# Kernel optimization log

Hardware: AMD Instinct MI355X
Metric: run time of the kernel (lower is better)

Reference implementation:

```python
import jax, jax.numpy as jnp
import numpy as np
import math

B, L, H, E, D = 4, 2048, 8, 64, 64
EPS = 1e-6

def _adjust(x):
    # signed power-law (sqrt) then L2-normalize over feature dim
    y = jnp.sign(x) * jnp.sqrt(jnp.abs(x) + EPS)
    return y / (jnp.linalg.norm(y, axis=-1, keepdims=True) + EPS)

def setup_inputs() -> dict:
    key = jax.random.key(0)
    kq, kk, kv, ka = jax.random.split(key, 4)
    queries = jax.random.normal(kq, (B, L, H, E), dtype=jnp.float32)
    keys = jax.random.normal(kk, (B, L, H, E), dtype=jnp.float32)
    values = jax.random.normal(kv, (B, L, H, D), dtype=jnp.float32)
    # TriangularCausalMask: True above the diagonal => masked
    attn_mask = jnp.triu(jnp.ones((1, 1, L, L), dtype=bool), k=1)
    alpha = jax.random.normal(ka, (1,), dtype=jnp.float32) * 0.01
    return {"queries": queries, "keys": keys, "values": values,
            "attn_mask": attn_mask, "alpha": alpha}

def reference(queries, keys, values, attn_mask, alpha):
    Bq, Lq, Hq, Eq = queries.shape
    scale = 1.0 / math.sqrt(Eq)
    # Closed form of torch.autograd.functional.jacobian of
    # sum(einsum('blhe,bshe->bhls', q, k)):
    #   d/dq[b,l,h,e] = sum_s k[b,s,h,e]   (independent of l)
    #   d/dk[b,s,h,e] = sum_l q[b,l,h,e]   (independent of s)
    k_sum = jnp.sum(keys, axis=1, keepdims=True)      # [B,1,H,E]
    q_sum = jnp.sum(queries, axis=1, keepdims=True)   # [B,1,H,E]
    q_adj = _adjust(queries + alpha * k_sum)
    k_adj = _adjust(keys + alpha * q_sum)
    scores = jnp.einsum('blhe,bshe->bhls', q_adj, k_adj)  # [B,H,L,S]
    scores = jnp.where(attn_mask, -jnp.inf, scores)
    A = jax.nn.softmax(scale * scores, axis=-1)  # dropout inactive (eval)
    V = jnp.einsum('bhls,bshd->blhd', A, values)
    return V
```

## Files before the change

### kernel.cpp

```cpp
#include <hip/hip_runtime.h>
#include <hip/hip_bf16.h>
#include <math.h>

#define NB 4
#define NL 2048
#define NH 8
#define NE 64
#define ND 64
#define EPSF 1e-6f
#define CEXP 0.180336881f

typedef __attribute__((ext_vector_type(8))) short bf16x8;
typedef __attribute__((ext_vector_type(4))) short s16x4;
typedef __attribute__((ext_vector_type(4))) float f32x4;

static __device__ __forceinline__ unsigned short bfbits(float x) {
  union { __hip_bfloat16 h; unsigned short u; } c;
  c.h = __float2bfloat16(x);
  return c.u;
}
static __device__ __forceinline__ float sgnsqrt(float x) {
  return x > 0.f ? sqrtf(x + EPSF) : (x < 0.f ? -sqrtf(-x + EPSF) : 0.f);
}

__global__ void sums_kernel(const float* __restrict__ q, const float* __restrict__ k,
                            float* __restrict__ pq, float* __restrict__ pk) {
  int bh = blockIdx.x, lp = blockIdx.y;
  int b = bh >> 3, h = bh & 7;
  int t = threadIdx.x;
  int eq = t & 15, lr = t >> 4;
  int wave = t >> 6, lane = t & 63;
  const float* qp = q + (((size_t)b * NL) * NH + h) * NE + eq * 4;
  const float* kp = k + (((size_t)b * NL) * NH + h) * NE + eq * 4;
  f32x4 aq = {0.f, 0.f, 0.f, 0.f}, ak = {0.f, 0.f, 0.f, 0.f};
#pragma unroll
  for (int i = 0; i < 8; ++i) {
    int l = lp * 128 + i * 16 + lr;
    size_t off = (size_t)l * NH * NE;
    aq += *(const f32x4*)(qp + off);
    ak += *(const f32x4*)(kp + off);
  }
#pragma unroll
  for (int c = 0; c < 4; ++c) {
    aq[c] += __shfl_xor(aq[c], 16, 64); aq[c] += __shfl_xor(aq[c], 32, 64);
    ak[c] += __shfl_xor(ak[c], 16, 64); ak[c] += __shfl_xor(ak[c], 32, 64);
  }
  __shared__ f32x4 sq[4][16], sk[4][16];
  if (lane < 16) { sq[wave][lane] = aq; sk[wave][lane] = ak; }
  __syncthreads();
  if (t < 16) {
    f32x4 s = sq[0][t] + sq[1][t] + sq[2][t] + sq[3][t];
    *(f32x4*)(pq + ((size_t)bh * 16 + lp) * 64 + t * 4) = s;
  } else if (t < 32) {
    int e = t - 16;
    f32x4 s = sk[0][e] + sk[1][e] + sk[2][e] + sk[3][e];
    *(f32x4*)(pk + ((size_t)bh * 16 + e < 0 ? 0 : ((size_t)bh * 16) + 0) * 0 + ((size_t)bh * 16 + lp) * 64 + e * 4) = s;
  }
}

__global__ void prep_kernel(const float* __restrict__ q, const float* __restrict__ k,
                            const float* __restrict__ v,
                            const float* __restrict__ pq, const float* __restrict__ pk,
                            const float* __restrict__ alpha,
                            __hip_bfloat16* __restrict__ qadj, __hip_bfloat16* __restrict__ kadj,
                            __hip_bfloat16* __restrict__ vt) {
  __shared__ float aqs[8][68], aks[8][68];
  __shared__ __hip_bfloat16 tile[64][68];
  int t = threadIdx.x;
  if (blockIdx.x < 1024) {
    int rid0 = blockIdx.x * 64;
    int b = rid0 >> 14;
    {
      int h = t >> 5, j = t & 31;
      const float* pqp = pq + ((size_t)(b * 8 + h) * 16) * 64 + j * 2;
      const float* pkp = pk + ((size_t)(b * 8 + h) * 16) * 64 + j * 2;
      float s0 = 0.f, s1 = 0.f, u0 = 0.f, u1 = 0.f;
#pragma unroll
      for (int lp = 0; lp < 16; ++lp) {
        s0 += pqp[lp * 64]; s1 += pqp[lp * 64 + 1];
        u0 += pkp[lp * 64]; u1 += pkp[lp * 64 + 1];
      }
      float al = alpha[0];
      aqs[h][j * 2] = al * s0; aqs[h][j * 2 + 1] = al * s1;
      aks[h][j * 2] = al * u0; aks[h][j * 2 + 1] = al * u1;
    }
    __syncthreads();
    int eq = t & 15, lr = t >> 4;
#pragma unroll
    for (int p = 0; p < 4; ++p) {
      int rid = rid0 + p * 16 + lr;
      int h = rid & 7, l = (rid >> 3) & 2047;
      f32x4 q4 = *(const f32x4*)(q + (size_t)rid * 64 + eq * 4);
      f32x4 k4 = *(const f32x4*)(k + (size_t)rid * 64 + eq * 4);
      f32x4 xq = q4 + *(const f32x4*)&aks[h][eq * 4];
      f32x4 xk = k4 + *(const f32x4*)&aqs[h][eq * 4];
      float yq[4], yk[4];
      float nq = 0.f, nk = 0.f;
#pragma unroll
      for (int c = 0; c < 4; ++c) {
        yq[c] = sgnsqrt(xq[c]); nq += yq[c] * yq[c];
        yk[c] = sgnsqrt(xk[c]); nk += yk[c] * yk[c];
      }
#pragma unroll
      for (int m = 1; m < 16; m <<= 1) {
        nq += __shfl_xor(nq, m, 16);
        nk += __shfl_xor(nk, m, 16);
      }
      float iq = 1.f / (sqrtf(nq) + EPSF);
      float ik = 1.f / (sqrtf(nk) + EPSF);
      s16x4 uq, uk;
#pragma unroll
      for (int c = 0; c < 4; ++c) {
        uq[c] = (short)bfbits(yq[c] * iq);
        uk[c] = (short)bfbits(yk[c] * ik);
      }
      size_t ooff = ((size_t)(b * 8 + h) * 2048 + l) * 64 + eq * 4;
      *(s16x4*)((char*)qadj + ooff * 2) = uq;
      *(s16x4*)((char*)kadj + ooff * 2) = uk;
    }
  } else {
    int blk = blockIdx.x - 1024;
    int s0 = (blk & 31) * 64;
    int bh = blk >> 5;
    int b = bh >> 3, h = bh & 7;
    {
      int sl = t >> 2, dg = t & 3;
      const float* src = v + (((size_t)b * NL + s0 + sl) * NH + h) * ND + dg * 16;
#pragma unroll
      for (int i = 0; i < 4; ++i) {
        f32x4 f = *(const f32x4*)(src + i * 4);
        tile[sl][dg * 16 + i * 4 + 0] = __float2bfloat16(f[0]);
        tile[sl][dg * 16 + i * 4 + 1] = __float2bfloat16(f[1]);
        tile[sl][dg * 16 + i * 4 + 2] = __float2bfloat16(f[2]);
        tile[sl][dg * 16 + i * 4 + 3] = __float2bfloat16(f[3]);
      }
    }
    __syncthreads();
    {
      int d = t >> 2, sg = t & 3;
      __align__(16) __hip_bfloat16 tmp[16];
#pragma unroll
      for (int i = 0; i < 16; ++i) {
        int c = sg * 16 + i;
        int blk32 = c >> 5, cc = c & 31;
        int cq = cc >> 2, ege = cq >> 1, hi = cq & 1;
        int s_local = blk32 * 32 + hi * 16 + ege * 4 + (cc & 3);
        tmp[i] = tile[s_local][d];
      }
      __hip_bfloat16* dst = vt + ((size_t)bh * ND + d) * NL + s0 + sg * 16;
      *(bf16x8*)(dst) = *(const bf16x8*)&tmp[0];
      *(bf16x8*)(dst + 8) = *(const bf16x8*)&tmp[8];
    }
  }
}

__global__ __launch_bounds__(256) void attn_kernel(const __hip_bfloat16* __restrict__ qadj,
                                                   const __hip_bfloat16* __restrict__ kadj,
                                                   const __hip_bfloat16* __restrict__ vt,
                                                   float* __restrict__ out) {
  __shared__ __align__(16) char lds[49152];
  int bh = blockIdx.x;
  int pairid = blockIdx.y;
  int b = bh >> 3, h = bh & 7;
  int wave = threadIdx.x >> 6, lane = threadIdx.x & 63;
  int qr = lane & 15, eg = lane >> 4;
  const char* kgb = (const char*)(kadj + (size_t)bh * NL * NE);
  const char* vgb = (const char*)(vt + (size_t)bh * ND * NL);
  const char* qgb = (const char*)(qadj + (size_t)bh * NL * NE);

  auto STAGE = [&](int bufsel, int ck) {
    char* dstbase = lds + bufsel * 16384;
    int s0 = ck * 64;
#pragma unroll
    for (int c = 0; c < 4; ++c) {
      int T = (wave * 4 + c) * 1024 + lane * 16;
      const char* src;
      if (T < 8192) {
        int S = T ^ (((T >> 7) & 7) << 4);
        src = kgb + (size_t)s0 * 128 + S;
      } else {
        int T2 = T - 8192;
        int S = T2 ^ (((T2 >> 7) & 7) << 4);
        int d = S >> 7, cc = S & 127;
        src = vgb + ((size_t)d * NL + s0) * 2 + cc;
      }
      __builtin_amdgcn_global_load_lds(
          (const __attribute__((address_space(1))) unsigned int*)src,
          (__attribute__((address_space(3))) unsigned int*)(dstbase + (wave * 4 + c) * 1024),
          16, 0, 0);
    }
  };

#pragma unroll 1
  for (int half = 0; half < 2; ++half) {
    int tile = half ? (31 - pairid) : pairid;
    int t0 = tile * 64;
    int nck = tile + 1;
    int qw0 = t0 + wave * 16;

    bf16x8 qf0 = *(const bf16x8*)(qgb + (size_t)(qw0 + qr) * 128 + eg * 16);
    bf16x8 qf1 = *(const bf16x8*)(qgb + (size_t)(qw0 + qr) * 128 + 64 + eg * 16);

    f32x4 acc[4];
#pragma unroll
    for (int dc = 0; dc < 4; ++dc) acc[dc] = (f32x4){0.f, 0.f, 0.f, 0.f};
    float srun = 0.f;

    if (half) {
      asm volatile("s_waitcnt vmcnt(0)" ::: "memory");
      __builtin_amdgcn_sched_barrier(0);
      __builtin_amdgcn_s_barrier();
    }
    STAGE(0, 0);
    if (nck > 1) STAGE(1, 1);

#pragma unroll 1
    for (int ck = 0; ck < nck; ++ck) {
      if (ck + 1 < nck) asm volatile("s_waitcnt vmcnt(4)" ::: "memory");
      else              asm volatile("s_waitcnt vmcnt(0)" ::: "memory");
      __builtin_amdgcn_sched_barrier(0);
      __builtin_amdgcn_s_barrier();
      __builtin_amdgcn_sched_barrier(0);
      if (ck + 2 < nck) STAGE((ck + 2) % 3, ck + 2);
      char* ldsK = lds + (ck % 3) * 16384;
      char* ldsV = ldsK + 8192;

      float p[4][4];
#pragma unroll
      for (int st = 0; st < 4; ++st) {
        f32x4 a = (f32x4){0.f, 0.f, 0.f, 0.f};
        int row = st * 16 + qr;
        int swz = (row & 7) << 4;
        bf16x8 k0 = *(const bf16x8*)(ldsK + ((row * 128 + eg * 16) ^ swz));
        bf16x8 k1 = *(const bf16x8*)(ldsK + ((row * 128 + 64 + eg * 16) ^ swz));
        a = __builtin_amdgcn_mfma_f32_16x16x32_bf16(k0, qf0, a, 0, 0, 0);
        a = __builtin_amdgcn_mfma_f32_16x16x32_bf16(k1, qf1, a, 0, 0, 0);
#pragma unroll
        for (int r = 0; r < 4; ++r) p[st][r] = a[r];
      }
      if (ck == nck - 1) {
#pragma unroll
        for (int st = 0; st < 4; ++st)
#pragma unroll
          for (int r = 0; r < 4; ++r)
            if (t0 + st * 16 + eg * 4 + r > qw0 + qr) p[st][r] = -1e30f;
      }
#pragma unroll
      for (int st = 0; st < 4; ++st)
#pragma unroll
        for (int r = 0; r < 4; ++r) p[st][r] = exp2f((p[st][r] - 1.0f) * CEXP);
      srun += ((p[0][0] + p[0][1] + p[0][2] + p[0][3]) + (p[1][0] + p[1][1] + p[1][2] + p[1][3])) +
              ((p[2][0] + p[2][1] + p[2][2] + p[2][3]) + (p[3][0] + p[3][1] + p[3][2] + p[3][3]));

#pragma unroll
      for (int pp = 0; pp < 2; ++pp) {
        bf16x8 pb;
#pragma unroll
        for (int j = 0; j < 4; ++j) {
          pb[j] = (short)bfbits(p[2 * pp][j]);
          pb[4 + j] = (short)bfbits(p[2 * pp + 1][j]);
        }
#pragma unroll
        for (int dc = 0; dc < 4; ++dc) {
          int d = dc * 16 + qr;
          bf16x8 vf = *(const bf16x8*)(ldsV + ((d * 128 + pp * 64 + eg * 16) ^ ((d & 7) << 4)));
          acc[dc] = __builtin_amdgcn_mfma_f32_16x16x32_bf16(vf, pb, acc[dc], 0, 0, 0);
        }
      }
    }

    srun += __shfl_xor(srun, 16, 64);
    srun += __shfl_xor(srun, 32, 64);
    float inv = 1.f / srun;
    int l = qw0 + qr;
    float* orow = out + (((size_t)b * NL + l) * NH + h) * ND;
#pragma unroll
    for (int dc = 0; dc < 4; ++dc) *(f32x4*)(orow + dc * 16 + eg * 4) = acc[dc] * inv;
  }
}

extern "C" void kernel_launch(void* const* d_in, const int* in_sizes, int n_in,
                              void* d_out, int out_size, void* d_ws, size_t ws_size,
                              hipStream_t stream) {
  const float* q = (const float*)d_in[0];
  const float* k = (const float*)d_in[1];
  const float* v = (const float*)d_in[2];
  const float* alpha = (const float*)d_in[4];
  float* out = (float*)d_out;
  char* ws = (char*)d_ws;

  __hip_bfloat16* qadj = (__hip_bfloat16*)(ws);
  __hip_bfloat16* kadj = (__hip_bfloat16*)(ws + 8388608);
  __hip_bfloat16* vt   = (__hip_bfloat16*)(ws + 16777216);
  float* pq = (float*)(ws + 25165824);
  float* pk = (float*)(ws + 25165824 + 131072);

  sums_kernel<<<dim3(32, 16), 256, 0, stream>>>(q, k, pq, pk);
  prep_kernel<<<dim3(2048), 256, 0, stream>>>(q, k, v, pq, pk, alpha, qadj, kadj, vt);
  attn_kernel<<<dim3(32, 16), 256, 0, stream>>>(qadj, kadj, vt, out);
}
```

Baseline: 162.8 us.

## Split attention work across key halves per wave with smaller query tiles

Restructures the attention kernel so each block handles a 32-row query tile instead of a pair of 64-row tiles. The four waves are split two by two across query halves and key-chunk halves, and the two key-half partial accumulators and row sums are combined through LDS at the end. The grid grows to four times as many blocks, launched heaviest tile first, LDS shrinks to a double buffer, and launch bounds request higher occupancy. LDS offsets are precomputed per thread. The cost is extra K/V restaging per query row and a full wait at every chunk instead of a three-deep pipeline.

```diff
diff --git a/kernel.cpp b/kernel.cpp
--- a/kernel.cpp
+++ b/kernel.cpp
@@ -54,7 +54,7 @@
   } else if (t < 32) {
     int e = t - 16;
     f32x4 s = sk[0][e] + sk[1][e] + sk[2][e] + sk[3][e];
-    *(f32x4*)(pk + ((size_t)bh * 16 + e < 0 ? 0 : ((size_t)bh * 16) + 0) * 0 + ((size_t)bh * 16 + lp) * 64 + e * 4) = s;
+    *(f32x4*)(pk + ((size_t)bh * 16 + lp) * 64 + e * 4) = s;
   }
 }
 
@@ -154,124 +154,141 @@
   }
 }
 
-__global__ __launch_bounds__(256) void attn_kernel(const __hip_bfloat16* __restrict__ qadj,
-                                                   const __hip_bfloat16* __restrict__ kadj,
-                                                   const __hip_bfloat16* __restrict__ vt,
-                                                   float* __restrict__ out) {
-  __shared__ __align__(16) char lds[49152];
+__global__ __launch_bounds__(256, 5) void attn_kernel(const __hip_bfloat16* __restrict__ qadj,
+                                                      const __hip_bfloat16* __restrict__ kadj,
+                                                      const __hip_bfloat16* __restrict__ vt,
+                                                      float* __restrict__ out) {
+  __shared__ __align__(16) char lds[32768];
   int bh = blockIdx.x;
-  int pairid = blockIdx.y;
+  int tile = 63 - (int)blockIdx.y;
   int b = bh >> 3, h = bh & 7;
   int wave = threadIdx.x >> 6, lane = threadIdx.x & 63;
   int qr = lane & 15, eg = lane >> 4;
+  int qhalf = wave >> 1, shalf = wave & 1;
+  int t0 = tile * 32;
+  int nck = (tile >> 1) + 1;
+  int qw0 = t0 + qhalf * 16;
   const char* kgb = (const char*)(kadj + (size_t)bh * NL * NE);
   const char* vgb = (const char*)(vt + (size_t)bh * ND * NL);
   const char* qgb = (const char*)(qadj + (size_t)bh * NL * NE);
 
+  int koff[2][2], voff[4];
+#pragma unroll
+  for (int st2 = 0; st2 < 2; ++st2) {
+    int row = shalf * 32 + st2 * 16 + qr;
+    int swz = (row & 7) << 4;
+    koff[st2][0] = (row * 128 + eg * 16) ^ swz;
+    koff[st2][1] = (row * 128 + 64 + eg * 16) ^ swz;
+  }
+#pragma unroll
+  for (int dc = 0; dc < 4; ++dc) {
+    int d = dc * 16 + qr;
+    voff[dc] = 8192 + ((d * 128 + shalf * 64 + eg * 16) ^ ((d & 7) << 4));
+  }
+  int src_off[4], dst_off[4];
+#pragma unroll
+  for (int c = 0; c < 4; ++c) {
+    dst_off[c] = (wave * 4 + c) * 1024;
+    if (wave < 2) {
+      int T = (wave * 4 + c) * 1024 + lane * 16;
+      src_off[c] = T ^ (((T >> 7) & 7) << 4);
+    } else {
+      int T2 = ((wave - 2) * 4 + c) * 1024 + lane * 16;
+      int S = T2 ^ (((T2 >> 7) & 7) << 4);
+      src_off[c] = (S >> 7) * (NL * 2) + (S & 127);
+    }
+  }
+  const char* sgb = (wave < 2) ? kgb : vgb;
+  int smul = (wave < 2) ? 8192 : 128;
+
   auto STAGE = [&](int bufsel, int ck) {
-    char* dstbase = lds + bufsel * 16384;
-    int s0 = ck * 64;
-#pragma unroll
-    for (int c = 0; c < 4; ++c) {
-      int T = (wave * 4 + c) * 1024 + lane * 16;
-      const char* src;
-      if (T < 8192) {
-        int S = T ^ (((T >> 7) & 7) << 4);
-        src = kgb + (size_t)s0 * 128 + S;
-      } else {
-        int T2 = T - 8192;
-        int S = T2 ^ (((T2 >> 7) & 7) << 4);
-        int d = S >> 7, cc = S & 127;
-        src = vgb + ((size_t)d * NL + s0) * 2 + cc;
-      }
+    const char* sb = sgb + (size_t)ck * smul;
+    char* db = lds + bufsel * 16384;
+#pragma unroll
+    for (int c = 0; c < 4; ++c)
       __builtin_amdgcn_global_load_lds(
-          (const __attribute__((address_space(1))) unsigned int*)src,
-          (__attribute__((address_space(3))) unsigned int*)(dstbase + (wave * 4 + c) * 1024),
+          (const __attribute__((address_space(1))) unsigned int*)(sb + src_off[c]),
+          (__attribute__((address_space(3))) unsigned int*)(db + dst_off[c]),
           16, 0, 0);
-    }
   };
 
+  bf16x8 qf0 = *(const bf16x8*)(qgb + (size_t)(qw0 + qr) * 128 + eg * 16);
+  bf16x8 qf1 = *(const bf16x8*)(qgb + (size_t)(qw0 + qr) * 128 + 64 + eg * 16);
+
+  f32x4 acc[4];
+#pragma unroll
+  for (int dc = 0; dc < 4; ++dc) acc[dc] = (f32x4){0.f, 0.f, 0.f, 0.f};
+  float srun = 0.f;
+
+  STAGE(0, 0);
 #pragma unroll 1
-  for (int half = 0; half < 2; ++half) {
-    int tile = half ? (31 - pairid) : pairid;
-    int t0 = tile * 64;
-    int nck = tile + 1;
-    int qw0 = t0 + wave * 16;
-
-    bf16x8 qf0 = *(const bf16x8*)(qgb + (size_t)(qw0 + qr) * 128 + eg * 16);
-    bf16x8 qf1 = *(const bf16x8*)(qgb + (size_t)(qw0 + qr) * 128 + 64 + eg * 16);
-
-    f32x4 acc[4];
-#pragma unroll
-    for (int dc = 0; dc < 4; ++dc) acc[dc] = (f32x4){0.f, 0.f, 0.f, 0.f};
-    float srun = 0.f;
-
-    if (half) {
-      asm volatile("s_waitcnt vmcnt(0)" ::: "memory");
-      __builtin_amdgcn_sched_barrier(0);
-      __builtin_amdgcn_s_barrier();
-    }
-    STAGE(0, 0);
-    if (nck > 1) STAGE(1, 1);
-
-#pragma unroll 1
-    for (int ck = 0; ck < nck; ++ck) {
-      if (ck + 1 < nck) asm volatile("s_waitcnt vmcnt(4)" ::: "memory");
-      else              asm volatile("s_waitcnt vmcnt(0)" ::: "memory");
-      __builtin_amdgcn_sched_barrier(0);
-      __builtin_amdgcn_s_barrier();
-      __builtin_amdgcn_sched_barrier(0);
-      if (ck + 2 < nck) STAGE((ck + 2) % 3, ck + 2);
-      char* ldsK = lds + (ck % 3) * 16384;
-      char* ldsV = ldsK + 8192;
-
-      float p[4][4];
-#pragma unroll
-      for (int st = 0; st < 4; ++st) {
-        f32x4 a = (f32x4){0.f, 0.f, 0.f, 0.f};
-        int row = st * 16 + qr;
-        int swz = (row & 7) << 4;
-        bf16x8 k0 = *(const bf16x8*)(ldsK + ((row * 128 + eg * 16) ^ swz));
-        bf16x8 k1 = *(const bf16x8*)(ldsK + ((row * 128 + 64 + eg * 16) ^ swz));
-        a = __builtin_amdgcn_mfma_f32_16x16x32_bf16(k0, qf0, a, 0, 0, 0);
-        a = __builtin_amdgcn_mfma_f32_16x16x32_bf16(k1, qf1, a, 0, 0, 0);
-#pragma unroll
-        for (int r = 0; r < 4; ++r) p[st][r] = a[r];
-      }
-      if (ck == nck - 1) {
-#pragma unroll
-        for (int st = 0; st < 4; ++st)
-#pragma unroll
-          for (int r = 0; r < 4; ++r)
-            if (t0 + st * 16 + eg * 4 + r > qw0 + qr) p[st][r] = -1e30f;
-      }
-#pragma unroll
-      for (int st = 0; st < 4; ++st)
-#pragma unroll
-        for (int r = 0; r < 4; ++r) p[st][r] = exp2f((p[st][r] - 1.0f) * CEXP);
-      srun += ((p[0][0] + p[0][1] + p[0][2] + p[0][3]) + (p[1][0] + p[1][1] + p[1][2] + p[1][3])) +
-              ((p[2][0] + p[2][1] + p[2][2] + p[2][3]) + (p[3][0] + p[3][1] + p[3][2] + p[3][3]));
-
-#pragma unroll
-      for (int pp = 0; pp < 2; ++pp) {
-        bf16x8 pb;
-#pragma unroll
-        for (int j = 0; j < 4; ++j) {
-          pb[j] = (short)bfbits(p[2 * pp][j]);
-          pb[4 + j] = (short)bfbits(p[2 * pp + 1][j]);
-        }
-#pragma unroll
-        for (int dc = 0; dc < 4; ++dc) {
-          int d = dc * 16 + qr;
-          bf16x8 vf = *(const bf16x8*)(ldsV + ((d * 128 + pp * 64 + eg * 16) ^ ((d & 7) << 4)));
-          acc[dc] = __builtin_amdgcn_mfma_f32_16x16x32_bf16(vf, pb, acc[dc], 0, 0, 0);
-        }
-      }
-    }
-
-    srun += __shfl_xor(srun, 16, 64);
-    srun += __shfl_xor(srun, 32, 64);
-    float inv = 1.f / srun;
+  for (int ck = 0; ck < nck; ++ck) {
+    asm volatile("s_waitcnt vmcnt(0)" ::: "memory");
+    __builtin_amdgcn_sched_barrier(0);
+    __builtin_amdgcn_s_barrier();
+    __builtin_amdgcn_sched_barrier(0);
+    if (ck + 1 < nck) STAGE((ck + 1) & 1, ck + 1);
+    char* base = lds + (ck & 1) * 16384;
+
+    float p[2][4];
+#pragma unroll
+    for (int st2 = 0; st2 < 2; ++st2) {
+      f32x4 a = (f32x4){0.f, 0.f, 0.f, 0.f};
+      bf16x8 k0 = *(const bf16x8*)(base + koff[st2][0]);
+      bf16x8 k1 = *(const bf16x8*)(base + koff[st2][1]);
+      a = __builtin_amdgcn_mfma_f32_16x16x32_bf16(k0, qf0, a, 0, 0, 0);
+      a = __builtin_amdgcn_mfma_f32_16x16x32_bf16(k1, qf1, a, 0, 0, 0);
+#pragma unroll
+      for (int r = 0; r < 4; ++r) p[st2][r] = a[r];
+    }
+    if (ck == nck - 1) {
+      int sbase = ck * 64 + shalf * 32 + eg * 4;
+      int qg = qw0 + qr;
+#pragma unroll
+      for (int st2 = 0; st2 < 2; ++st2)
+#pragma unroll
+        for (int r = 0; r < 4; ++r)
+          if (sbase + st2 * 16 + r > qg) p[st2][r] = -1e30f;
+    }
+#pragma unroll
+    for (int st2 = 0; st2 < 2; ++st2)
+#pragma unroll
+      for (int r = 0; r < 4; ++r) p[st2][r] = exp2f((p[st2][r] - 1.0f) * CEXP);
+    srun += ((p[0][0] + p[0][1]) + (p[0][2] + p[0][3])) +
+            ((p[1][0] + p[1][1]) + (p[1][2] + p[1][3]));
+
+    bf16x8 pb;
+#pragma unroll
+    for (int j = 0; j < 4; ++j) {
+      pb[j] = (short)bfbits(p[0][j]);
+      pb[4 + j] = (short)bfbits(p[1][j]);
+    }
+#pragma unroll
+    for (int dc = 0; dc < 4; ++dc) {
+      bf16x8 vf = *(const bf16x8*)(base + voff[dc]);
+      acc[dc] = __builtin_amdgcn_mfma_f32_16x16x32_bf16(vf, pb, acc[dc], 0, 0, 0);
+    }
+  }
+
+  srun += __shfl_xor(srun, 16, 64);
+  srun += __shfl_xor(srun, 32, 64);
+  __syncthreads();
+  if (shalf == 1) {
+    float* m = (float*)(lds + qhalf * 4352 + lane * 68);
+#pragma unroll
+    for (int dc = 0; dc < 4; ++dc)
+#pragma unroll
+      for (int r = 0; r < 4; ++r) m[dc * 4 + r] = acc[dc][r];
+    m[16] = srun;
+  }
+  __syncthreads();
+  if (shalf == 0) {
+    const float* m = (const float*)(lds + qhalf * 4352 + lane * 68);
+#pragma unroll
+    for (int dc = 0; dc < 4; ++dc)
+#pragma unroll
+      for (int r = 0; r < 4; ++r) acc[dc][r] += m[dc * 4 + r];
+    float inv = 1.f / (srun + m[16]);
     int l = qw0 + qr;
     float* orow = out + (((size_t)b * NL + l) * NH + h) * ND;
 #pragma unroll
@@ -297,5 +314,5 @@
 
   sums_kernel<<<dim3(32, 16), 256, 0, stream>>>(q, k, pq, pk);
   prep_kernel<<<dim3(2048), 256, 0, stream>>>(q, k, v, pq, pk, alpha, qadj, kadj, vt);
-  attn_kernel<<<dim3(32, 16), 256, 0, stream>>>(qadj, kadj, vt, out);
-}
+  attn_kernel<<<dim3(32, 64), 256, 0, stream>>>(qadj, kadj, vt, out);
+}
```

Result: faster. 151.7 us (-6.8%).
